# Optimization experiments

Hardware: AMD Instinct MI355X
Metric: run time of the kernel (lower is better)

The kernel has to match this reference:

```python
import jax, jax.numpy as jnp
import numpy as np

B, S, D = 1, 2048, 2048
H, DH = 16, 128
GEMMA2_TANH_SCALE = 50.0


def _rotate_half(x):
    x1, x2 = jnp.split(x, 2, axis=-1)
    return jnp.concatenate([-x2, x1], axis=-1)


def setup_inputs() -> dict:
    key = jax.random.key(0)
    ks = jax.random.split(key, 8)
    x = jax.random.normal(ks[0], (B, S, D), dtype=jnp.float32)
    # rotary tables per position: cos/sin of theta_i duplicated over half-dim pairs
    inv_freq = 1.0 / (10000.0 ** (jnp.arange(0, DH // 2, dtype=jnp.float32) / (DH // 2)))
    t = jnp.arange(S, dtype=jnp.float32)
    freqs = jnp.einsum('s,d->sd', t, inv_freq)          # [S, DH/2]
    emb = jnp.concatenate([freqs, freqs], axis=-1)       # [S, DH]
    rope_cos = jnp.cos(emb)
    rope_sin = jnp.sin(emb)
    # causal additive mask [1,1,S,S]
    neg = jnp.float32(-1e9)
    mask = jnp.where(jnp.tril(jnp.ones((S, S), dtype=bool)), 0.0, neg)[None, None]
    scale = 1.0 / np.sqrt(D)
    wq = jax.random.normal(ks[1], (H * DH, D), dtype=jnp.float32) * scale
    wk = jax.random.normal(ks[2], (H * DH, D), dtype=jnp.float32) * scale
    wv = jax.random.normal(ks[3], (H * DH, D), dtype=jnp.float32) * scale
    wo = jax.random.normal(ks[4], (D, H * DH), dtype=jnp.float32) * scale
    return {"x": x, "rope_cos": rope_cos, "rope_sin": rope_sin, "mask": mask,
            "wq": wq, "wk": wk, "wv": wv, "wo": wo}


def reference(x, rope_cos, rope_sin, mask, wq, wk, wv, wo):
    b, s, _ = x.shape
    xq = jnp.einsum('bsd,pd->bsp', x, wq).reshape(b, s, H, DH)
    xk = jnp.einsum('bsd,pd->bsp', x, wk).reshape(b, s, H, DH)
    xv = jnp.einsum('bsd,pd->bsp', x, wv).reshape(b, s, H, DH)
    cos = rope_cos[None, :, None, :]  # [1,S,1,DH]
    sin = rope_sin[None, :, None, :]
    xq = xq * cos + _rotate_half(xq) * sin
    xk = xk * cos + _rotate_half(xk) * sin
    q = xq.transpose(0, 2, 1, 3)  # [B,H,S,DH]
    k = xk.transpose(0, 2, 1, 3)
    v = xv.transpose(0, 2, 1, 3)
    scores = jnp.einsum('bhqd,bhkd->bhqk', q, k) / np.sqrt(DH)
    scores = jnp.tanh(scores / GEMMA2_TANH_SCALE) * GEMMA2_TANH_SCALE
    scores = scores + mask
    probs = jax.nn.softmax(scores.astype(jnp.float32), axis=-1).astype(q.dtype)
    out = jnp.einsum('bhqk,bhkd->bhqd', probs, v)
    out = out.transpose(0, 2, 1, 3).reshape(b, s, H * DH)
    return jnp.einsum('bsp,dp->bsd', out, wo)
```

## Files before the change

### kernel.cpp

```cpp
#include <hip/hip_runtime.h>

#define SS 2048
#define DD 2048
#define HH 16
#define DHD 128

#define SCORE_SCALE 0.08838834764831845f
#define C2 0.0035355339059327377f

typedef unsigned short u16;
typedef __attribute__((ext_vector_type(8))) short short8;
typedef __attribute__((ext_vector_type(4))) short short4v;
typedef __attribute__((ext_vector_type(4))) float f32x4;

__device__ __forceinline__ float bf2f(u16 v) {
  union { unsigned u; float f; } x; x.u = ((unsigned)v) << 16; return x.f;
}
__device__ __forceinline__ u16 f2bf(float f) {
  union { float f; unsigned u; } x; x.f = f;
  unsigned r = (x.u + 0x7fffu + ((x.u >> 16) & 1u)) >> 16;
  return (u16)r;
}

#define GL2LDS16(g, l) __builtin_amdgcn_global_load_lds( \
    (const __attribute__((address_space(1))) void*)(g),   \
    (__attribute__((address_space(3))) void*)(l), 16, 0, 0)

__global__ __launch_bounds__(256) void cvt5(const float* __restrict__ i0,
                                            const float* __restrict__ i1,
                                            const float* __restrict__ i2,
                                            const float* __restrict__ i3,
                                            const float* __restrict__ i4,
                                            u16* __restrict__ o0, u16* __restrict__ o1,
                                            u16* __restrict__ o2, u16* __restrict__ o3,
                                            u16* __restrict__ o4) {
  const int z = blockIdx.y;
  const float* in = (z == 0) ? i0 : (z == 1) ? i1 : (z == 2) ? i2 : (z == 3) ? i3 : i4;
  u16* out = (z == 0) ? o0 : (z == 1) ? o1 : (z == 2) ? o2 : (z == 3) ? o3 : o4;
  int i = (blockIdx.x * 256 + threadIdx.x) * 8;
  float4 a = *(const float4*)(in + i);
  float4 b = *(const float4*)(in + i + 4);
  short8 o;
  o[0] = (short)f2bf(a.x); o[1] = (short)f2bf(a.y);
  o[2] = (short)f2bf(a.z); o[3] = (short)f2bf(a.w);
  o[4] = (short)f2bf(b.x); o[5] = (short)f2bf(b.y);
  o[6] = (short)f2bf(b.z); o[7] = (short)f2bf(b.w);
  *(short8*)(out + i) = o;
}


#define GEMM_STAGE(Asrc, Bsrc, Adst, Bdst, kofs)                               \
  _Pragma("unroll")                                                            \
  for (int half = 0; half < 2; ++half) {                                       \
    const int rb = half * 64 + wave * 16;                                      \
    GL2LDS16(Asrc + (size_t)(bm + rb + lrow) * DD + (kofs) + c8s, Adst + rb * 32); \
    GL2LDS16(Bsrc + (size_t)(bn + rb + lrow) * DD + (kofs) + c8s, Bdst + rb * 32); \
  }

#define GEMM_COMPUTE(Abuf, Bbuf)                                               \
  {                                                                            \
    short8 af[4], bb[4];                                                       \
    _Pragma("unroll")                                                          \
    for (int m = 0; m < 4; ++m) {                                              \
      const int row = wm + m * 16 + fr;                                        \
      af[m] = *(const short8*)(Abuf + row * 32 + (hi ^ ((row >> 1) & 3)) * 8); \
    }                                                                          \
    _Pragma("unroll")                                                          \
    for (int n = 0; n < 4; ++n) {                                              \
      const int row = wn + n * 16 + fr;                                        \
      bb[n] = *(const short8*)(Bbuf + row * 32 + (hi ^ ((row >> 1) & 3)) * 8); \
    }                                                                          \
    __builtin_amdgcn_s_setprio(1);                                             \
    _Pragma("unroll")                                                          \
    for (int m = 0; m < 4; ++m)                                                \
      _Pragma("unroll")                                                        \
      for (int n = 0; n < 4; ++n)                                              \
        acc[m][n] = __builtin_amdgcn_mfma_f32_16x16x32_bf16(af[m], bb[n], acc[m][n], 0, 0, 0); \
    __builtin_amdgcn_s_setprio(0);                                             \
  }

#define GEMM_KLOOP(A_, B_)                                                     \
  GEMM_STAGE(A_, B_, As0, Bs0, 0)                                              \
  __syncthreads();                                                             \
  for (int kk = 0; kk < DD / 32; kk += 2) {                                    \
    if (kk + 1 < DD / 32) { GEMM_STAGE(A_, B_, As1, Bs1, (kk + 1) * 32) }      \
    GEMM_COMPUTE(As0, Bs0)                                                     \
    __syncthreads();                                                           \
    if (kk + 2 < DD / 32) { GEMM_STAGE(A_, B_, As0, Bs0, (kk + 2) * 32) }      \
    GEMM_COMPUTE(As1, Bs1)                                                     \
    __syncthreads();                                                           \
  }

__global__ __launch_bounds__(256) void gemm_bt(const u16* __restrict__ A,
                                               const u16* __restrict__ B,
                                               float* __restrict__ C) {
  __shared__ u16 smem[16384];
  u16* As0 = smem;            u16* As1 = smem + 4096;
  u16* Bs0 = smem + 8192;     u16* Bs1 = smem + 12288;
  const int tid = threadIdx.x, wave = tid >> 6, lane = tid & 63;
  const int wm = (wave >> 1) * 64, wn = (wave & 1) * 64;
  const int bm = blockIdx.y * 128, bn = blockIdx.x * 128;
  const int lrow = lane >> 2;
  const int c8s = ((lane & 3) ^ ((lrow >> 1) & 3)) * 8;
  const int fr = lane & 15, hi = lane >> 4, fq4 = hi * 4;
  f32x4 acc[4][4] = {};
  GEMM_KLOOP(A, B)
#pragma unroll
  for (int m = 0; m < 4; ++m)
#pragma unroll
    for (int n = 0; n < 4; ++n) {
      const int row0 = bm + wm + m * 16 + fq4;
      const int col  = bn + wn + n * 16 + fr;
#pragma unroll
      for (int r = 0; r < 4; ++r)
        C[(size_t)(row0 + r) * DD + col] = acc[m][n][r];
    }
}

__global__ __launch_bounds__(256) void gemm_qkv(const u16* __restrict__ A,
                                                const u16* __restrict__ Bq,
                                                const u16* __restrict__ Bk,
                                                const u16* __restrict__ Bv,
                                                u16* __restrict__ Cq,
                                                u16* __restrict__ Ck,
                                                u16* __restrict__ Cvt) {
  __shared__ u16 smem[16384];
  u16* As0 = smem;            u16* As1 = smem + 4096;
  u16* Bs0 = smem + 8192;     u16* Bs1 = smem + 12288;
  const int z = blockIdx.z;
  const u16* B = (z == 0) ? Bq : (z == 1) ? Bk : Bv;
  const int tid = threadIdx.x, wave = tid >> 6, lane = tid & 63;
  const int wm = (wave >> 1) * 64, wn = (wave & 1) * 64;
  const int bm = blockIdx.y * 128, bn = blockIdx.x * 128;
  const int lrow = lane >> 2;
  const int c8s = ((lane & 3) ^ ((lrow >> 1) & 3)) * 8;
  const int fr = lane & 15, hi = lane >> 4, fq4 = hi * 4;
  f32x4 acc[4][4] = {};
  GEMM_KLOOP(A, B)
  u16* Cn = (z == 0) ? Cq : Ck;
#pragma unroll
  for (int m = 0; m < 4; ++m)
#pragma unroll
    for (int n = 0; n < 4; ++n) {
      const int row0 = bm + wm + m * 16 + fq4;
      const int col  = bn + wn + n * 16 + fr;
      if (z < 2) {
#pragma unroll
        for (int r = 0; r < 4; ++r)
          Cn[(size_t)(row0 + r) * DD + col] = f2bf(acc[m][n][r]);
      } else {
        short4v t;
#pragma unroll
        for (int r = 0; r < 4; ++r) t[r] = (short)f2bf(acc[m][n][r]);
        *(short4v*)(Cvt + (size_t)col * SS + row0) = t;
      }
    }
}

__global__ __launch_bounds__(256) void rope2(const u16* __restrict__ qin,
                                             const u16* __restrict__ kin,
                                             const float* __restrict__ cosd,
                                             const float* __restrict__ sind,
                                             u16* __restrict__ qt,
                                             u16* __restrict__ kt) {
  const int e = (blockIdx.x * 256 + threadIdx.x) * 8;
  const int s = e >> 11, col = e & 2047;
  const int h = col >> 7, d = col & 127;
  const float sgn = (d & 64) ? 1.0f : -1.0f;
  short8 qa = *(const short8*)(qin + e);
  short8 qp = *(const short8*)(qin + (e ^ 64));
  short8 ka = *(const short8*)(kin + e);
  short8 kp = *(const short8*)(kin + (e ^ 64));
  f32x4 c0 = *(const f32x4*)(cosd + s * DHD + d);
  f32x4 c1 = *(const f32x4*)(cosd + s * DHD + d + 4);
  f32x4 s0 = *(const f32x4*)(sind + s * DHD + d);
  f32x4 s1 = *(const f32x4*)(sind + s * DHD + d + 4);
  short8 oq, ok;
#pragma unroll
  for (int j = 0; j < 8; ++j) {
    const float c = (j < 4) ? c0[j] : c1[j - 4];
    const float sn = (j < 4) ? s0[j] : s1[j - 4];
    oq[j] = (short)f2bf(bf2f((u16)qa[j]) * c + sgn * bf2f((u16)qp[j]) * sn);
    ok[j] = (short)f2bf(bf2f((u16)ka[j]) * c + sgn * bf2f((u16)kp[j]) * sn);
  }
  const size_t o = ((size_t)h * SS + s) * DHD + d;
  *(short8*)(qt + o) = oq;
  *(short8*)(kt + o) = ok;
}

__global__ __launch_bounds__(256) void attn_fwd(const u16* __restrict__ qt,
                                                const u16* __restrict__ kt,
                                                const u16* __restrict__ vt,
                                                u16* __restrict__ ao) {
  __shared__ u16 Ks[2][64 * 128];
  __shared__ u16 Vs[2][128 * 64];
  __shared__ u16 Ps[4][16 * 64];
  const int bid = blockIdx.x;
  const int h  = (bid & 7) + 8 * ((bid >> 3) & 1);
  const int qb = (SS / 64 - 1) - (bid >> 4);
  const int tid = threadIdx.x, wave = tid >> 6, lane = tid & 63;
  const int q0 = qb * 64 + wave * 16;
  const int fr = lane & 15, hi = lane >> 4, fq8 = hi * 8, fq4 = hi * 4;

  const int kbrow0 = wave * 4 + (lane >> 4);
  const int kc8    = (lane & 15);
  const int vbrow0 = wave * 8 + (lane >> 3);
  const int vk8    = (lane & 7) ^ ((lane >> 3) & 7);

  short8 qf[4];
#pragma unroll
  for (int c = 0; c < 4; ++c)
    qf[c] = *(const short8*)(qt + ((size_t)h * SS + q0 + fr) * DHD + c * 32 + fq8);

  f32x4 oacc[8] = {};
  float lsum[4] = {0.f, 0.f, 0.f, 0.f};

  const int nt = qb + 1;

  auto STAGE = [&](int t, int buf) {
    const int kb = t * 64;
#pragma unroll
    for (int i = 0; i < 4; ++i) {
      const int krow = i * 16 + kbrow0;
      const int c8 = kc8 ^ (krow & 7);
      GL2LDS16(kt + ((size_t)h * SS + kb + krow) * DHD + c8 * 8,
               &Ks[buf][(i * 16 + wave * 4) * 128]);
    }
#pragma unroll
    for (int i = 0; i < 4; ++i) {
      const int vrow = i * 32 + vbrow0;
      GL2LDS16(vt + ((size_t)h * DHD + vrow) * SS + kb + vk8 * 8,
               &Vs[buf][(i * 32 + wave * 8) * 64]);
    }
  };

  STAGE(0, 0);
  __syncthreads();

  for (int t = 0; t < nt; ++t) {
    const int buf = t & 1;
    if (t + 1 < nt) STAGE(t + 1, buf ^ 1);
    const int kb = t * 64;

    f32x4 sacc[4] = {};
    __builtin_amdgcn_s_setprio(1);
#pragma unroll
    for (int n = 0; n < 4; ++n) {
      const int row = n * 16 + fr;
#pragma unroll
      for (int c = 0; c < 4; ++c) {
        short8 b = *(const short8*)(&Ks[buf][row * 128 + ((c * 4 + hi) ^ (fr & 7)) * 8]);
        sacc[n] = __builtin_amdgcn_mfma_f32_16x16x32_bf16(qf[c], b, sacc[n], 0, 0, 0);
      }
    }
    __builtin_amdgcn_s_setprio(0);

    const bool diag = (t == nt - 1);
    float p[4][4];
#pragma unroll
    for (int n = 0; n < 4; ++n)
#pragma unroll
      for (int r = 0; r < 4; ++r) {
        const float w = __expf(sacc[n][r] * C2);
        float pv = __expf(-100.0f * __builtin_amdgcn_rcpf(1.0f + w));
        if (diag) {
          const int kg = kb + n * 16 + fr;
          if (kg > q0 + fq4 + r) pv = 0.0f;
        }
        p[n][r] = pv;
        lsum[r] += pv;
      }

    u16* ps = &Ps[wave][0];
#pragma unroll
    for (int n = 0; n < 4; ++n)
#pragma unroll
      for (int r = 0; r < 4; ++r) {
        const int prow = fq4 + r;
        const int chunk = n * 2 + (fr >> 3);
        ps[prow * 64 + ((chunk ^ (prow & 7)) << 3) + (fr & 7)] = f2bf(p[n][r]);
      }
    short8 pa[2];
#pragma unroll
    for (int kc = 0; kc < 2; ++kc)
      pa[kc] = *(const short8*)(ps + fr * 64 + (((kc * 4 + hi) ^ (fr & 7)) << 3));

    __builtin_amdgcn_s_setprio(1);
#pragma unroll
    for (int kc = 0; kc < 2; ++kc)
#pragma unroll
      for (int n = 0; n < 8; ++n) {
        const int row = n * 16 + fr;
        short8 b = *(const short8*)(&Vs[buf][row * 64 + (((kc * 4 + hi) ^ (fr & 7)) << 3)]);
        oacc[n] = __builtin_amdgcn_mfma_f32_16x16x32_bf16(pa[kc], b, oacc[n], 0, 0, 0);
      }
    __builtin_amdgcn_s_setprio(0);
    __syncthreads();
  }

  float rl[4];
#pragma unroll
  for (int r = 0; r < 4; ++r) {
    float v = lsum[r];
    v += __shfl_xor(v, 1); v += __shfl_xor(v, 2);
    v += __shfl_xor(v, 4); v += __shfl_xor(v, 8);
    rl[r] = 1.0f / v;
  }
#pragma unroll
  for (int n = 0; n < 8; ++n)
#pragma unroll
    for (int r = 0; r < 4; ++r) {
      const float v = oacc[n][r] * rl[r];
      ao[(size_t)(q0 + fq4 + r) * DD + h * DHD + n * 16 + fr] = f2bf(v);
    }
}

extern "C" void kernel_launch(void* const* d_in, const int* in_sizes, int n_in,
                              void* d_out, int out_size, void* d_ws, size_t ws_size,
                              hipStream_t stream) {
  const float* x        = (const float*)d_in[0];
  const float* rope_cos = (const float*)d_in[1];
  const float* rope_sin = (const float*)d_in[2];
  const float* wq = (const float*)d_in[4];
  const float* wk = (const float*)d_in[5];
  const float* wv = (const float*)d_in[6];
  const float* wo = (const float*)d_in[7];
  float* out = (float*)d_out;

  u16* ws = (u16*)d_ws;
  const size_t SZ = (size_t)SS * DD;
  u16* xb  = ws + 0 * SZ;
  u16* wqb = ws + 1 * SZ;
  u16* wkb = ws + 2 * SZ;
  u16* wvb = ws + 3 * SZ;
  u16* wob = ws + 4 * SZ;
  u16* q_  = ws + 5 * SZ;
  u16* k_  = ws + 6 * SZ;
  u16* vt  = ws + 7 * SZ;
  u16* qt  = wqb;
  u16* kt  = wkb;
  u16* ao  = wvb;

  cvt5<<<dim3((int)(SZ / (256 * 8)), 5), 256, 0, stream>>>(
      x, wq, wk, wv, wo, xb, wqb, wkb, wvb, wob);

  gemm_qkv<<<dim3(16, 16, 3), 256, 0, stream>>>(
      xb, wqb, wkb, wvb, q_, k_, vt);

  rope2<<<(int)(SZ / (256 * 8)), 256, 0, stream>>>(
      q_, k_, rope_cos, rope_sin, qt, kt);

  attn_fwd<<<512, 256, 0, stream>>>(qt, kt, vt, ao);

  gemm_bt<<<dim3(16, 16), 256, 0, stream>>>(ao, wob, out);
}
```

Measured before the change: 298.3 us.

## Split output projection GEMM K dimension across two wave groups per block

The output projection GEMM now launches 512-thread blocks in which two groups of four waves each handle half of the K=2048 reduction, using separate double-buffered LDS regions. The second group writes its partial accumulators to LDS and the first group adds them before storing to global memory. The goal is more waves in flight for a grid of only 256 blocks, which underfills the GPU. The cost is double the LDS per block, which limits occupancy, plus an extra LDS reduction pass.

Result: faster. 281.9 us (-5.5%).

```diff
diff --git a/kernel.cpp b/kernel.cpp
--- a/kernel.cpp
+++ b/kernel.cpp
@@ -91,30 +91,62 @@
     __syncthreads();                                                           \
   }
 
-__global__ __launch_bounds__(256) void gemm_bt(const u16* __restrict__ A,
-                                               const u16* __restrict__ B,
-                                               float* __restrict__ C) {
-  __shared__ u16 smem[16384];
-  u16* As0 = smem;            u16* As1 = smem + 4096;
-  u16* Bs0 = smem + 8192;     u16* Bs1 = smem + 12288;
-  const int tid = threadIdx.x, wave = tid >> 6, lane = tid & 63;
+__global__ __launch_bounds__(512) void gemm_bt_sk(const u16* __restrict__ A,
+                                                  const u16* __restrict__ B,
+                                                  float* __restrict__ C) {
+  __shared__ u16 smem[33792];
+  const int tid = threadIdx.x;
+  const int wave8 = tid >> 6, lane = tid & 63;
+  const int gq = wave8 >> 2;
+  const int wave = wave8 & 3;
   const int wm = (wave >> 1) * 64, wn = (wave & 1) * 64;
   const int bm = blockIdx.y * 128, bn = blockIdx.x * 128;
   const int lrow = lane >> 2;
   const int c8s = ((lane & 3) ^ ((lrow >> 1) & 3)) * 8;
   const int fr = lane & 15, hi = lane >> 4, fq4 = hi * 4;
+  u16* base = smem + gq * 16384;
+  u16* As0 = base;            u16* As1 = base + 4096;
+  u16* Bs0 = base + 8192;     u16* Bs1 = base + 12288;
+  const int k0 = gq * 1024;
   f32x4 acc[4][4] = {};
-  GEMM_KLOOP(A, B)
-#pragma unroll
-  for (int m = 0; m < 4; ++m)
-#pragma unroll
-    for (int n = 0; n < 4; ++n) {
-      const int row0 = bm + wm + m * 16 + fq4;
-      const int col  = bn + wn + n * 16 + fr;
-#pragma unroll
-      for (int r = 0; r < 4; ++r)
-        C[(size_t)(row0 + r) * DD + col] = acc[m][n][r];
-    }
+  GEMM_STAGE(A, B, As0, Bs0, k0)
+  __syncthreads();
+  for (int kk = 0; kk < 32; kk += 2) {
+    if (kk + 1 < 32) { GEMM_STAGE(A, B, As1, Bs1, k0 + (kk + 1) * 32) }
+    GEMM_COMPUTE(As0, Bs0)
+    __syncthreads();
+    if (kk + 2 < 32) { GEMM_STAGE(A, B, As0, Bs0, k0 + (kk + 2) * 32) }
+    GEMM_COMPUTE(As1, Bs1)
+    __syncthreads();
+  }
+  float* red = (float*)smem;
+  if (gq == 1) {
+#pragma unroll
+    for (int m = 0; m < 4; ++m)
+#pragma unroll
+      for (int n = 0; n < 4; ++n) {
+        const int lr0 = wm + m * 16 + fq4;
+        const int lc  = wn + n * 16 + fr;
+#pragma unroll
+        for (int r = 0; r < 4; ++r)
+          red[(lr0 + r) * 132 + lc] = acc[m][n][r];
+      }
+  }
+  __syncthreads();
+  if (gq == 0) {
+#pragma unroll
+    for (int m = 0; m < 4; ++m)
+#pragma unroll
+      for (int n = 0; n < 4; ++n) {
+        const int row0 = bm + wm + m * 16 + fq4;
+        const int col  = bn + wn + n * 16 + fr;
+        const int lr0 = wm + m * 16 + fq4;
+        const int lc  = wn + n * 16 + fr;
+#pragma unroll
+        for (int r = 0; r < 4; ++r)
+          C[(size_t)(row0 + r) * DD + col] = acc[m][n][r] + red[(lr0 + r) * 132 + lc];
+      }
+  }
 }
 
 __global__ __launch_bounds__(256) void gemm_qkv(const u16* __restrict__ A,
@@ -352,5 +384,5 @@
 
   attn_fwd<<<512, 256, 0, stream>>>(qt, kt, vt, ao);
 
-  gemm_bt<<<dim3(16, 16), 256, 0, stream>>>(ao, wob, out);
-}
+  gemm_bt_sk<<<dim3(16, 16), 512, 0, stream>>>(ao, wob, out);
+}
```
